# Performance work log

Hardware: AMD Instinct MI355X
Metric: run time of the kernel (lower is better)

## Reference

```python
import math
import jax, jax.numpy as jnp
import numpy as np

H = 16  # number of heads

def setup_inputs() -> dict:
    key0 = jax.random.key(0)
    ks = jax.random.split(key0, 8)
    B, S, D = 4, 2048, 1024
    query = jax.random.normal(ks[0], (B, S, D), dtype=jnp.float32)
    key_t = jax.random.normal(ks[1], (B, S, D), dtype=jnp.float32)
    value = jax.random.normal(ks[2], (B, S, D), dtype=jnp.float32)
    mask = jax.random.randint(ks[3], (B, S, S), 0, 2, dtype=jnp.int32)
    scale = 1.0 / math.sqrt(D)
    Wq = jax.random.normal(ks[4], (D, D), dtype=jnp.float32) * scale
    Wk = jax.random.normal(ks[5], (D, D), dtype=jnp.float32) * scale
    Wv = jax.random.normal(ks[6], (D, D), dtype=jnp.float32) * scale
    Wo = jax.random.normal(ks[7], (D, D), dtype=jnp.float32) * scale
    return {"query": query, "key": key_t, "value": value, "mask": mask,
            "Wq": Wq, "Wk": Wk, "Wv": Wv, "Wo": Wo}


def reference(query, key, value, mask, Wq, Wk, Wv, Wo):
    B, S, D = query.shape
    dk = D // H
    # Linear projections (nn.Linear, no bias): x @ W.T, then split heads
    def proj(x, W):
        return (x @ W.T).reshape(B, -1, H, dk).transpose(0, 2, 1, 3)  # [B,H,S,dk]
    q = proj(query, Wq)
    k = proj(key, Wk)
    v = proj(value, Wv)
    scores = jnp.einsum('bhqd,bhkd->bhqk', q, k) / math.sqrt(dk)
    m = mask[:, None, :, :] != 0  # [B,1,Sq,Sk] broadcast over heads
    scores = jnp.where(m, scores, jnp.float32(-1e9))
    p = jax.nn.softmax(scores, axis=-1)
    p = jnp.where(m, p, 0.0)
    # dropout is identity in eval mode
    x = jnp.einsum('bhqk,bhkd->bhqd', p, v)
    x = x.transpose(0, 2, 1, 3).reshape(B, -1, D)
    return x @ Wo.T
```

## Files before the change

kernel.cpp:

```cpp
#include <hip/hip_runtime.h>
#include <hip/hip_bf16.h>
#include <stdint.h>
#include <stddef.h>

typedef __bf16 bf16_t;
typedef __bf16 bf16x8 __attribute__((ext_vector_type(8)));
typedef __bf16 bf16x4 __attribute__((ext_vector_type(4)));
typedef float floatx4 __attribute__((ext_vector_type(4)));

#define D_MODEL 1024
#define SEQ 2048
#define NB 4
#define NH 16
#define DK 64
#define MTOT 8192

#define QSCALE 0.1803368801111204f
#define FMAX 14.0f

__device__ inline bf16x8 ld8f(const float* p) {
  float4 a = *(const float4*)p;
  float4 b = *(const float4*)(p + 4);
  bf16x8 v;
  v[0] = (bf16_t)a.x; v[1] = (bf16_t)a.y; v[2] = (bf16_t)a.z; v[3] = (bf16_t)a.w;
  v[4] = (bf16_t)b.x; v[5] = (bf16_t)b.y; v[6] = (bf16_t)b.z; v[7] = (bf16_t)b.w;
  return v;
}

typedef const __attribute__((address_space(1))) unsigned int gu32;
typedef __attribute__((address_space(3))) unsigned int lu32;
__device__ static inline void async_copy16(const void* g, void* l) {
  __builtin_amdgcn_global_load_lds((gu32*)g, (lu32*)l, 16, 0, 0);
}

__global__ __launch_bounds__(256) void cvt_kernel(
    const float* __restrict__ q, const float* __restrict__ k,
    const float* __restrict__ v, const float* __restrict__ Wq,
    const float* __restrict__ Wk, const float* __restrict__ Wv,
    bf16_t* __restrict__ qb, bf16_t* __restrict__ kb, bf16_t* __restrict__ vb,
    bf16_t* __restrict__ wqb, bf16_t* __restrict__ wkb,
    bf16_t* __restrict__ wvb) {
  size_t c = (size_t)blockIdx.x * 256 + threadIdx.x;
  const float* src;
  bf16_t* dst;
  size_t off;
  if (c < 1048576) { src = q; dst = qb; off = c; }
  else if (c < 2097152) { src = k; dst = kb; off = c - 1048576; }
  else if (c < 3145728) { src = v; dst = vb; off = c - 2097152; }
  else if (c < 3276800) { src = Wq; dst = wqb; off = c - 3145728; }
  else if (c < 3407872) { src = Wk; dst = wkb; off = c - 3276800; }
  else { src = Wv; dst = wvb; off = c - 3407872; }
  size_t e = off * 8;
  *(bf16x8*)&dst[e] = ld8f(&src[e]);
}

__global__ __launch_bounds__(256) void cvt_w_kernel(const float* __restrict__ W,
                                                    bf16_t* __restrict__ wb) {
  size_t e = ((size_t)blockIdx.x * 256 + threadIdx.x) * 8;
  *(bf16x8*)&wb[e] = ld8f(&W[e]);
}

__global__ __launch_bounds__(256) void mask_bits_kernel(
    const int* __restrict__ mask, uint32_t* __restrict__ bits) {
  const int lane = threadIdx.x & 63;
  const size_t w0 = ((size_t)blockIdx.x * blockDim.x + threadIdx.x) >> 6;
  const size_t nw = ((size_t)gridDim.x * blockDim.x) >> 6;
  const size_t total = (size_t)NB * SEQ * SEQ / 64;
  for (size_t i = w0; i < total; i += nw) {
    int v = mask[i * 64 + lane];
    unsigned long long b = __ballot(v != 0);
    if (lane == 0) *(unsigned long long*)&bits[i * 2] = b;
  }
}

#define BM 128
#define BN 128
#define BK 64

template <int MODE, typename TC>
__global__ __launch_bounds__(256) void gemm_bt(const bf16_t* __restrict__ A,
                                               const bf16_t* __restrict__ W,
                                               TC* __restrict__ C, float scale) {
  __shared__ __align__(16) bf16_t As[BM * BK];
  __shared__ __align__(16) bf16_t Bs[BN * BK];
  const int tid = threadIdx.x;
  const int lane = tid & 63;
  const int wave = tid >> 6;
  const int row0 = blockIdx.x * BM;
  const int col0 = blockIdx.y * BN;
  const int wr = (wave >> 1) * 64;
  const int wc = (wave & 1) * 64;
  const int lrow = lane & 15;
  const int quad = lane >> 4;
  const int srow = lane >> 3;
  const int scol = ((lane & 7) ^ srow) * 8;

  floatx4 acc[4][4] = {};

  for (int k0 = 0; k0 < D_MODEL; k0 += BK) {
#pragma unroll
    for (int it = 0; it < 4; it++) {
      int seg = wave * 4 + it;
      async_copy16(&A[(size_t)(row0 + seg * 8 + srow) * D_MODEL + k0 + scol],
                   &As[seg * 512]);
      async_copy16(&W[(size_t)(col0 + seg * 8 + srow) * D_MODEL + k0 + scol],
                   &Bs[seg * 512]);
    }
    __syncthreads();
#pragma unroll
    for (int kk = 0; kk < BK; kk += 32) {
      bf16x8 af[4], bfr[4];
#pragma unroll
      for (int i = 0; i < 4; i++)
        af[i] = *(const bf16x8*)&As[(wr + i * 16 + lrow) * BK +
                                    (((kk >> 3) + quad) ^ (lane & 7)) * 8];
#pragma unroll
      for (int j = 0; j < 4; j++)
        bfr[j] = *(const bf16x8*)&Bs[(wc + j * 16 + lrow) * BK +
                                     (((kk >> 3) + quad) ^ (lane & 7)) * 8];
#pragma unroll
      for (int i = 0; i < 4; i++)
#pragma unroll
        for (int j = 0; j < 4; j++)
          acc[i][j] = __builtin_amdgcn_mfma_f32_16x16x32_bf16(af[i], bfr[j],
                                                              acc[i][j], 0, 0, 0);
    }
    __syncthreads();
  }

#pragma unroll
  for (int i = 0; i < 4; i++) {
#pragma unroll
    for (int j = 0; j < 4; j++) {
      int gr0 = row0 + wr + i * 16 + quad * 4;
      int gc = col0 + wc + j * 16 + lrow;
      if (MODE == 1) {
        int b = gr0 >> 11;
        int s = gr0 & (SEQ - 1);
        bf16x4 v;
#pragma unroll
        for (int r = 0; r < 4; r++) v[r] = (bf16_t)(acc[i][j][r] * scale);
        *(bf16x4*)&C[((size_t)(b * D_MODEL + gc)) * SEQ + s] = v;
      } else {
#pragma unroll
        for (int r = 0; r < 4; r++)
          C[(size_t)(gr0 + r) * D_MODEL + gc] = (TC)(acc[i][j][r] * scale);
      }
    }
  }
}

#define LP 136

__global__ __launch_bounds__(256) void attn_kernel(
    const bf16_t* __restrict__ Q, const bf16_t* __restrict__ K,
    const bf16_t* __restrict__ Vt, const uint32_t* __restrict__ bits,
    bf16_t* __restrict__ X) {
  __shared__ __align__(16) bf16_t Ps[64 * LP];
  __shared__ __align__(16) bf16_t Ks[128 * DK];
  __shared__ __align__(16) bf16_t Vs[DK * 128];
  const int tid = threadIdx.x;
  const int lane = tid & 63;
  const int wave = tid >> 6;
  const int lrow = lane & 15;
  const int quad = lane >> 4;
  const int bh = blockIdx.x & 63;
  const int qbase = (blockIdx.x >> 6) * 64;
  const int b = bh >> 4;
  const int h = bh & 15;
  const int q0w = qbase + wave * 16;
  const int srow8 = lane >> 3;
  const int scol8 = ((lane & 7) ^ srow8) * 8;
  const int vrow = lane >> 4;

  bf16x8 qf[2];
#pragma unroll
  for (int ks = 0; ks < 2; ks++)
    qf[ks] = *(const bf16x8*)&Q[((size_t)(b * SEQ + q0w + lrow)) * D_MODEL +
                                h * DK + ks * 32 + quad * 8];

  bf16x8 ones;
#pragma unroll
  for (int e = 0; e < 8; e++) ones[e] = (bf16_t)1.0f;

  floatx4 O[4] = {};
  floatx4 lsum = {};

  for (int kt = 0; kt < SEQ / 128; kt++) {
    const int kbase = kt * 128;
    uint32_t mw[4][4];
#pragma unroll
    for (int r = 0; r < 4; r++)
      *(uint4*)&mw[r][0] =
          *(const uint4*)&bits[((size_t)(b * SEQ + q0w + quad * 4 + r)) * 64 +
                               kt * 4];
    __syncthreads();
#pragma unroll
    for (int it = 0; it < 4; it++) {
      int seg = wave * 4 + it;
      async_copy16(&K[((size_t)(b * SEQ + kbase + seg * 8 + srow8)) * D_MODEL +
                      h * DK + scol8],
                   &Ks[seg * 512]);
    }
#pragma unroll
    for (int it = 0; it < 4; it++) {
      int seg = wave * 4 + it;
      int d = seg * 4 + vrow;
      async_copy16(&Vt[((size_t)(b * D_MODEL + h * DK + d)) * SEQ + kbase +
                       ((lrow ^ (d & 15)) * 8)],
                   &Vs[seg * 512]);
    }
    __syncthreads();

    floatx4 s[8];
#pragma unroll
    for (int kj = 0; kj < 8; kj++) {
      s[kj][0] = -FMAX; s[kj][1] = -FMAX; s[kj][2] = -FMAX; s[kj][3] = -FMAX;
#pragma unroll
      for (int ks = 0; ks < 2; ks++) {
        bf16x8 kf = *(const bf16x8*)&Ks[(kj * 16 + lrow) * DK +
                                        (((4 * ks + quad) ^ (lrow & 7)) * 8)];
        s[kj] = __builtin_amdgcn_mfma_f32_16x16x32_bf16(qf[ks], kf, s[kj], 0, 0, 0);
      }
    }

#pragma unroll
    for (int r = 0; r < 4; r++) {
#pragma unroll
      for (int kj = 0; kj < 8; kj++) {
        uint32_t ws = mw[r][kj >> 1] >> lrow;
        uint32_t ok = (kj & 1) ? (ws >> 16) & 1u : ws & 1u;
        float p = exp2f(s[kj][r]);
        p = ok ? p : 0.f;
        Ps[(wave * 16 + quad * 4 + r) * LP + kj * 16 + lrow] = (bf16_t)p;
      }
    }
    asm volatile("s_waitcnt lgkmcnt(0)" ::: "memory");

#pragma unroll
    for (int ks = 0; ks < 4; ks++) {
      bf16x8 pf =
          *(const bf16x8*)&Ps[(wave * 16 + lrow) * LP + ks * 32 + quad * 8];
#pragma unroll
      for (int dj = 0; dj < 4; dj++) {
        int vr = dj * 16 + lrow;
        bf16x8 vf = *(const bf16x8*)&Vs[vr * 128 +
                                        (((4 * ks + quad) ^ lrow) * 8)];
        O[dj] = __builtin_amdgcn_mfma_f32_16x16x32_bf16(pf, vf, O[dj], 0, 0, 0);
      }
      lsum = __builtin_amdgcn_mfma_f32_16x16x32_bf16(pf, ones, lsum, 0, 0, 0);
    }
  }

#pragma unroll
  for (int r = 0; r < 4; r++) {
    int qrow = q0w + quad * 4 + r;
    float li = lsum[r];
    float inv = (li > 0.f) ? 1.f / li : 0.f;
#pragma unroll
    for (int dj = 0; dj < 4; dj++)
      X[((size_t)(b * SEQ + qrow)) * D_MODEL + h * DK + dj * 16 + lrow] =
          (bf16_t)(O[dj][r] * inv);
  }
}

extern "C" void kernel_launch(void* const* d_in, const int* in_sizes, int n_in,
                              void* d_out, int out_size, void* d_ws,
                              size_t ws_size, hipStream_t stream) {
  const float* query = (const float*)d_in[0];
  const float* key = (const float*)d_in[1];
  const float* value = (const float*)d_in[2];
  const int* mask = (const int*)d_in[3];
  const float* Wq = (const float*)d_in[4];
  const float* Wk = (const float*)d_in[5];
  const float* Wv = (const float*)d_in[6];
  const float* Wo = (const float*)d_in[7];
  float* out = (float*)d_out;

  char* ws = (char*)d_ws;
  char* dob = (char*)d_out;
  bf16_t* qb = (bf16_t*)(ws);
  bf16_t* kb = (bf16_t*)(ws + ((size_t)16 << 20));
  bf16_t* vb = (bf16_t*)(ws + ((size_t)32 << 20));
  bf16_t* Kp = qb;
  bf16_t* Vtp = kb;
  bf16_t* Xp = vb;
  bf16_t* wob = (bf16_t*)ws;
  bf16_t* Qp = (bf16_t*)d_out;
  uint32_t* bits = (uint32_t*)(dob + ((size_t)16 << 20));
  bf16_t* wqb = (bf16_t*)(dob + ((size_t)18 << 20));
  bf16_t* wkb = (bf16_t*)(dob + ((size_t)20 << 20));
  bf16_t* wvb = (bf16_t*)(dob + ((size_t)22 << 20));

  cvt_kernel<<<13824, 256, 0, stream>>>(query, key, value, Wq, Wk, Wv, qb, kb,
                                        vb, wqb, wkb, wvb);
  mask_bits_kernel<<<2048, 256, 0, stream>>>(mask, bits);

  dim3 gg(MTOT / BM, D_MODEL / BN);
  gemm_bt<0, bf16_t><<<gg, 256, 0, stream>>>(qb, wqb, Qp, QSCALE);
  gemm_bt<0, bf16_t><<<gg, 256, 0, stream>>>(kb, wkb, Kp, 1.0f);
  gemm_bt<1, bf16_t><<<gg, 256, 0, stream>>>(vb, wvb, Vtp, 1.0f);
  attn_kernel<<<dim3(SEQ / 64 * NB * NH), 256, 0, stream>>>(Qp, Kp, Vtp, bits,
                                                            Xp);
  cvt_w_kernel<<<512, 256, 0, stream>>>(Wo, wob);
  gemm_bt<0, float><<<gg, 256, 0, stream>>>(Xp, wob, out, 1.0f);
}
```

Before: 450.7 us.

## Rewrite attention with 32x32 MFMA and register-resident P via permlane swap

The attention kernel moves from 16x16x32 to 32x32x16 MFMA tiles, computing S transposed (K as the A operand) so the probabilities stay in registers. They are packed to bf16 with v_cvt_pk_bf16_f32 and rearranged with v_permlane32_swap, removing the shared-memory P buffer and its write/read round trip. Each block now covers 128 queries, halving the grid and the K/V tile loads per query. It depends on gfx950-specific instructions and a correct register layout mapping, and uses more accumulator registers per thread.

```diff
diff --git a/kernel.cpp b/kernel.cpp
--- a/kernel.cpp
+++ b/kernel.cpp
@@ -7,6 +7,7 @@
 typedef __bf16 bf16x8 __attribute__((ext_vector_type(8)));
 typedef __bf16 bf16x4 __attribute__((ext_vector_type(4)));
 typedef float floatx4 __attribute__((ext_vector_type(4)));
+typedef float floatx16 __attribute__((ext_vector_type(16)));
 
 #define D_MODEL 1024
 #define SEQ 2048
@@ -31,6 +32,12 @@
 typedef __attribute__((address_space(3))) unsigned int lu32;
 __device__ static inline void async_copy16(const void* g, void* l) {
   __builtin_amdgcn_global_load_lds((gu32*)g, (lu32*)l, 16, 0, 0);
+}
+
+__device__ static inline uint32_t cvtpk_bf16(float lo, float hi) {
+  uint32_t r;
+  asm("v_cvt_pk_bf16_f32 %0, %1, %2" : "=v"(r) : "v"(lo), "v"(hi));
+  return r;
 }
 
 __global__ __launch_bounds__(256) void cvt_kernel(
@@ -150,50 +157,47 @@
   }
 }
 
-#define LP 136
-
 __global__ __launch_bounds__(256) void attn_kernel(
     const bf16_t* __restrict__ Q, const bf16_t* __restrict__ K,
     const bf16_t* __restrict__ Vt, const uint32_t* __restrict__ bits,
     bf16_t* __restrict__ X) {
-  __shared__ __align__(16) bf16_t Ps[64 * LP];
   __shared__ __align__(16) bf16_t Ks[128 * DK];
   __shared__ __align__(16) bf16_t Vs[DK * 128];
   const int tid = threadIdx.x;
   const int lane = tid & 63;
   const int wave = tid >> 6;
-  const int lrow = lane & 15;
-  const int quad = lane >> 4;
+  const int l31 = lane & 31;
+  const int half = lane >> 5;
+  const int lrow16 = lane & 15;
   const int bh = blockIdx.x & 63;
-  const int qbase = (blockIdx.x >> 6) * 64;
+  const int qbase = (blockIdx.x >> 6) * 128;
   const int b = bh >> 4;
   const int h = bh & 15;
-  const int q0w = qbase + wave * 16;
+  const int q0w = qbase + wave * 32;
   const int srow8 = lane >> 3;
   const int scol8 = ((lane & 7) ^ srow8) * 8;
   const int vrow = lane >> 4;
 
-  bf16x8 qf[2];
-#pragma unroll
-  for (int ks = 0; ks < 2; ks++)
-    qf[ks] = *(const bf16x8*)&Q[((size_t)(b * SEQ + q0w + lrow)) * D_MODEL +
-                                h * DK + ks * 32 + quad * 8];
+  bf16x8 qf[4];
+#pragma unroll
+  for (int kst = 0; kst < 4; kst++)
+    qf[kst] = *(const bf16x8*)&Q[((size_t)(b * SEQ + q0w + l31)) * D_MODEL +
+                                 h * DK + kst * 16 + half * 8];
 
   bf16x8 ones;
 #pragma unroll
   for (int e = 0; e < 8; e++) ones[e] = (bf16_t)1.0f;
 
-  floatx4 O[4] = {};
-  floatx4 lsum = {};
+  const int kfbase = (l31 * 64) ^ ((lane & 7) * 8) ^ (half * 8);
+  const int vfbase = (l31 * 128) ^ (lrow16 * 8) ^ (half * 8);
+
+  floatx16 O0 = {}, O1 = {}, lsum = {};
 
   for (int kt = 0; kt < SEQ / 128; kt++) {
     const int kbase = kt * 128;
-    uint32_t mw[4][4];
-#pragma unroll
-    for (int r = 0; r < 4; r++)
-      *(uint4*)&mw[r][0] =
-          *(const uint4*)&bits[((size_t)(b * SEQ + q0w + quad * 4 + r)) * 64 +
-                               kt * 4];
+    const uint4 m4 =
+        *(const uint4*)&bits[((size_t)(b * SEQ + q0w + l31)) * 64 + kt * 4];
+    const uint32_t mwa[4] = {m4.x, m4.y, m4.z, m4.w};
     __syncthreads();
 #pragma unroll
     for (int it = 0; it < 4; it++) {
@@ -207,60 +211,58 @@
       int seg = wave * 4 + it;
       int d = seg * 4 + vrow;
       async_copy16(&Vt[((size_t)(b * D_MODEL + h * DK + d)) * SEQ + kbase +
-                       ((lrow ^ (d & 15)) * 8)],
+                       ((lrow16 ^ (d & 15)) * 8)],
                    &Vs[seg * 512]);
     }
     __syncthreads();
 
-    floatx4 s[8];
-#pragma unroll
-    for (int kj = 0; kj < 8; kj++) {
-      s[kj][0] = -FMAX; s[kj][1] = -FMAX; s[kj][2] = -FMAX; s[kj][3] = -FMAX;
+#pragma unroll
+    for (int t = 0; t < 4; t++) {
+      floatx16 s;
+#pragma unroll
+      for (int r = 0; r < 16; r++) s[r] = -FMAX;
+#pragma unroll
+      for (int kst = 0; kst < 4; kst++) {
+        bf16x8 kf =
+            *(const bf16x8*)&Ks[t * 2048 + (kfbase ^ (kst * 16))];
+        s = __builtin_amdgcn_mfma_f32_32x32x16_bf16(kf, qf[kst], s, 0, 0, 0);
+      }
+      const uint32_t wh = mwa[t] >> (half * 4);
+#pragma unroll
+      for (int r = 0; r < 16; r++) {
+        float p = exp2f(s[r]);
+        s[r] = ((wh >> ((r & 3) + 8 * (r >> 2))) & 1u) ? p : 0.f;
+      }
 #pragma unroll
       for (int ks = 0; ks < 2; ks++) {
-        bf16x8 kf = *(const bf16x8*)&Ks[(kj * 16 + lrow) * DK +
-                                        (((4 * ks + quad) ^ (lrow & 7)) * 8)];
-        s[kj] = __builtin_amdgcn_mfma_f32_16x16x32_bf16(qf[ks], kf, s[kj], 0, 0, 0);
+        uint32_t w0 = cvtpk_bf16(s[8 * ks + 0], s[8 * ks + 1]);
+        uint32_t w2 = cvtpk_bf16(s[8 * ks + 4], s[8 * ks + 5]);
+        uint32_t w1 = cvtpk_bf16(s[8 * ks + 2], s[8 * ks + 3]);
+        uint32_t w3 = cvtpk_bf16(s[8 * ks + 6], s[8 * ks + 7]);
+        asm("v_permlane32_swap_b32 %0, %1" : "+v"(w0), "+v"(w2));
+        asm("v_permlane32_swap_b32 %0, %1" : "+v"(w1), "+v"(w3));
+        union { uint32_t u[4]; bf16x8 v; } pa;
+        pa.u[0] = w0; pa.u[1] = w1; pa.u[2] = w2; pa.u[3] = w3;
+        bf16x8 vf0 =
+            *(const bf16x8*)&Vs[vfbase ^ (t * 32 + ks * 16)];
+        bf16x8 vf1 =
+            *(const bf16x8*)&Vs[4096 + (vfbase ^ (t * 32 + ks * 16))];
+        O0 = __builtin_amdgcn_mfma_f32_32x32x16_bf16(pa.v, vf0, O0, 0, 0, 0);
+        O1 = __builtin_amdgcn_mfma_f32_32x32x16_bf16(pa.v, vf1, O1, 0, 0, 0);
+        lsum = __builtin_amdgcn_mfma_f32_32x32x16_bf16(pa.v, ones, lsum, 0, 0, 0);
       }
     }
-
-#pragma unroll
-    for (int r = 0; r < 4; r++) {
-#pragma unroll
-      for (int kj = 0; kj < 8; kj++) {
-        uint32_t ws = mw[r][kj >> 1] >> lrow;
-        uint32_t ok = (kj & 1) ? (ws >> 16) & 1u : ws & 1u;
-        float p = exp2f(s[kj][r]);
-        p = ok ? p : 0.f;
-        Ps[(wave * 16 + quad * 4 + r) * LP + kj * 16 + lrow] = (bf16_t)p;
-      }
-    }
-    asm volatile("s_waitcnt lgkmcnt(0)" ::: "memory");
-
-#pragma unroll
-    for (int ks = 0; ks < 4; ks++) {
-      bf16x8 pf =
-          *(const bf16x8*)&Ps[(wave * 16 + lrow) * LP + ks * 32 + quad * 8];
-#pragma unroll
-      for (int dj = 0; dj < 4; dj++) {
-        int vr = dj * 16 + lrow;
-        bf16x8 vf = *(const bf16x8*)&Vs[vr * 128 +
-                                        (((4 * ks + quad) ^ lrow) * 8)];
-        O[dj] = __builtin_amdgcn_mfma_f32_16x16x32_bf16(pf, vf, O[dj], 0, 0, 0);
-      }
-      lsum = __builtin_amdgcn_mfma_f32_16x16x32_bf16(pf, ones, lsum, 0, 0, 0);
-    }
-  }
-
-#pragma unroll
-  for (int r = 0; r < 4; r++) {
-    int qrow = q0w + quad * 4 + r;
+  }
+
+#pragma unroll
+  for (int r = 0; r < 16; r++) {
+    int qrow = q0w + (r & 3) + 8 * (r >> 2) + 4 * half;
     float li = lsum[r];
     float inv = (li > 0.f) ? 1.f / li : 0.f;
-#pragma unroll
-    for (int dj = 0; dj < 4; dj++)
-      X[((size_t)(b * SEQ + qrow)) * D_MODEL + h * DK + dj * 16 + lrow] =
-          (bf16_t)(O[dj][r] * inv);
+    X[((size_t)(b * SEQ + qrow)) * D_MODEL + h * DK + l31] =
+        (bf16_t)(O0[r] * inv);
+    X[((size_t)(b * SEQ + qrow)) * D_MODEL + h * DK + 32 + l31] =
+        (bf16_t)(O1[r] * inv);
   }
 }
 
@@ -300,8 +302,8 @@
   gemm_bt<0, bf16_t><<<gg, 256, 0, stream>>>(qb, wqb, Qp, QSCALE);
   gemm_bt<0, bf16_t><<<gg, 256, 0, stream>>>(kb, wkb, Kp, 1.0f);
   gemm_bt<1, bf16_t><<<gg, 256, 0, stream>>>(vb, wvb, Vtp, 1.0f);
-  attn_kernel<<<dim3(SEQ / 64 * NB * NH), 256, 0, stream>>>(Qp, Kp, Vtp, bits,
-                                                            Xp);
+  attn_kernel<<<dim3(SEQ / 128 * NB * NH), 256, 0, stream>>>(Qp, Kp, Vtp, bits,
+                                                             Xp);
   cvt_w_kernel<<<512, 256, 0, stream>>>(Wo, wob);
   gemm_bt<0, float><<<gg, 256, 0, stream>>>(Xp, wob, out, 1.0f);
 }
```

Result: faster. 433.7 us (-3.8%).
